# Kernel optimization log

Measured on AMD Instinct MI355X. Metric: run time of the kernel, lower is better.

Reference implementation:

```python
import jax, jax.numpy as jnp
import numpy as np
import math

# FPN level specs: (H, W, stride, anchor_size) for an 800x1216 input image
LEVELS = [(200, 304, 4, 32), (100, 152, 8, 64), (50, 76, 16, 128), (25, 38, 32, 256), (13, 19, 64, 512)]
RATIOS = (0.5, 1.0, 2.0)
A = 3
IMG_H, IMG_W = 800, 1216
PRE_NMS_TOPK = 1000   # test-time per level
POST_NMS_TOPK = 1000  # test-time
NMS_THRESH = 0.7
SCALE_CLAMP = math.log(1000.0 / 16)
NEG_INF = -1e9


def grid_anchors(H, W, stride, size):
    # detectron2 generate_cell_anchors: area=size^2, w=sqrt(area/r), h=w*r, centered at 0
    ca = []
    for r in RATIOS:
        w = math.sqrt(size * size / r)
        h = w * r
        ca.append([-w / 2.0, -h / 2.0, w / 2.0, h / 2.0])
    ca = np.asarray(ca, np.float32)                      # [A,4]
    sx = np.arange(W, dtype=np.float32) * stride
    sy = np.arange(H, dtype=np.float32) * stride
    yy, xx = np.meshgrid(sy, sx, indexing="ij")
    shifts = np.stack([xx, yy, xx, yy], -1).reshape(-1, 1, 4)  # [H*W,1,4]
    return jnp.asarray((shifts + ca[None]).reshape(-1, 4))      # [H*W*A,4]


def conv(x, w, b, pad):
    y = jax.lax.conv_general_dilated(x, w, (1, 1), [(pad, pad), (pad, pad)],
                                     dimension_numbers=("NCHW", "OIHW", "NCHW"))
    return y + b[None, :, None, None]


def apply_deltas(deltas, boxes):
    # Box2BoxTransform.apply_deltas with weights (1,1,1,1)
    w = boxes[..., 2] - boxes[..., 0]
    h = boxes[..., 3] - boxes[..., 1]
    cx = boxes[..., 0] + 0.5 * w
    cy = boxes[..., 1] + 0.5 * h
    dx, dy = deltas[..., 0], deltas[..., 1]
    dw = jnp.minimum(deltas[..., 2], SCALE_CLAMP)
    dh = jnp.minimum(deltas[..., 3], SCALE_CLAMP)
    pcx = dx * w + cx
    pcy = dy * h + cy
    pw = jnp.exp(dw) * w
    ph = jnp.exp(dh) * h
    return jnp.stack([pcx - 0.5 * pw, pcy - 0.5 * ph, pcx + 0.5 * pw, pcy + 0.5 * ph], -1)


def iou_one_vs_all(b, boxes):
    lt = jnp.maximum(b[:2], boxes[:, :2])
    rb = jnp.minimum(b[2:], boxes[:, 2:])
    wh = jnp.clip(rb - lt, 0.0)
    inter = wh[:, 0] * wh[:, 1]
    a1 = (b[2] - b[0]) * (b[3] - b[1])
    a2 = (boxes[:, 2] - boxes[:, 0]) * (boxes[:, 3] - boxes[:, 1])
    return inter / jnp.maximum(a1 + a2 - inter, 1e-9)


def nms_fixed(boxes, scores):
    # Fixed-iteration greedy NMS: POST_NMS_TOPK selections, jit-friendly.
    def body(scores_w, _):
        i = jnp.argmax(scores_w)
        s = scores_w[i]
        valid = s > NEG_INF / 2
        b = boxes[i]
        supp = iou_one_vs_all(b, boxes) > NMS_THRESH
        new_scores = jnp.where(supp, NEG_INF, scores_w)
        out_box = jnp.where(valid, b, jnp.zeros_like(b))
        out_s = jnp.where(valid, s, NEG_INF)
        return new_scores, (out_box, out_s)

    _, (kb, ks) = jax.lax.scan(body, scores, None, length=POST_NMS_TOPK)
    return kb, ks  # [K,4], [K]


def rpn_forward(feats, conv_w, conv_b, obj_w, obj_b, delta_w, delta_b):
    all_b, all_s = [], []
    for feat, (H, W, stride, size) in zip(feats, LEVELS):
        N = feat.shape[0]
        t = jax.nn.relu(conv(feat, conv_w, conv_b, 1))
        logits = conv(t, obj_w, obj_b, 0)                 # [N,A,H,W]
        deltas = conv(t, delta_w, delta_b, 0)             # [N,4A,H,W]
        logits = logits.transpose(0, 2, 3, 1).reshape(N, -1)                       # [N,HWA]
        deltas = deltas.reshape(N, A, 4, H, W).transpose(0, 3, 4, 1, 2).reshape(N, -1, 4)
        anch = grid_anchors(H, W, stride, size)           # [HWA,4]
        k = min(PRE_NMS_TOPK, H * W * A)
        s, idx = jax.lax.top_k(logits, k)                 # per-level pre-NMS topk
        d = jnp.take_along_axis(deltas, idx[..., None], axis=1)
        a = anch[idx]
        boxes = apply_deltas(d, a)
        boxes = jnp.stack([boxes[..., 0].clip(0, IMG_W), boxes[..., 1].clip(0, IMG_H),
                           boxes[..., 2].clip(0, IMG_W), boxes[..., 3].clip(0, IMG_H)], -1)
        all_b.append(boxes)
        all_s.append(s)
    boxes = jnp.concatenate(all_b, 1)   # [N,M,4]
    scores = jnp.concatenate(all_s, 1)  # [N,M]
    valid = ((boxes[..., 2] - boxes[..., 0]) > 0.0) & ((boxes[..., 3] - boxes[..., 1]) > 0.0)
    scores_m = jnp.where(valid, scores, NEG_INF)
    kb, ks = jax.vmap(nms_fixed)(boxes, scores_m)
    return jnp.concatenate([kb, ks[..., None]], -1)  # [N, POST_NMS_TOPK, 5]


def setup_inputs() -> dict:
    key = jax.random.key(0)
    ks = jax.random.split(key, 9)
    inp = {}
    for i, (name, (H, W, _, _)) in enumerate(zip(["feat_p2", "feat_p3", "feat_p4", "feat_p5", "feat_p6"], LEVELS)):
        inp[name] = jax.random.normal(ks[i], (2, 256, H, W), jnp.float32)
    inp["conv_w"] = jax.random.normal(ks[5], (256, 256, 3, 3), jnp.float32) * 0.02
    inp["conv_b"] = jnp.zeros((256,), jnp.float32)
    inp["obj_w"] = jax.random.normal(ks[6], (3, 256, 1, 1), jnp.float32) * 0.05
    inp["obj_b"] = jnp.zeros((3,), jnp.float32)
    inp["delta_w"] = jax.random.normal(ks[7], (12, 256, 1, 1), jnp.float32) * 0.02
    inp["delta_b"] = jnp.zeros((12,), jnp.float32)
    return inp


def reference(feat_p2, feat_p3, feat_p4, feat_p5, feat_p6, conv_w, conv_b, obj_w, obj_b, delta_w, delta_b):
    feats = [feat_p2, feat_p3, feat_p4, feat_p5, feat_p6]
    return rpn_forward(feats, conv_w, conv_b, obj_w, obj_b, delta_w, delta_b)
```

## Files before the change

### kernel.cpp

```cpp
#include <hip/hip_runtime.h>
#include <math.h>

typedef unsigned int u32;
typedef unsigned long long u64;
typedef __attribute__((ext_vector_type(8))) short bf16x8;
typedef __attribute__((ext_vector_type(4))) float f32x4;
typedef __attribute__((ext_vector_type(4))) double f64x4;

__constant__ int c_W[5]   = {304,152,76,38,19};
__constant__ int c_H[5]   = {200,100,50,25,13};
__constant__ int c_STR[5] = {4,8,16,32,64};
__constant__ int c_SZ[5]  = {32,64,128,256,512};
__constant__ int c_S[5]   = {182400,45600,11400,2850,741};
__constant__ int c_K1[5]  = {1024,1024,1024,1024,741};
__constant__ int c_K2[5]  = {1000,1000,1000,1000,741};
__constant__ u64 c_SCOFF[5] = {0,364800,456000,478800,484500};
__constant__ int c_LOFF[5] = {0,1000,2000,3000,4000};
__constant__ int c_PRE[6] = {0,2000,2600,2800,2850,2876};
__constant__ int c_NX[5]  = {5,3,2,1,1};

static const size_t h_SCOFF[5] = {0,364800,456000,478800,484500};

static constexpr size_t alignup(size_t x){ return (x + 255) & ~(size_t)255; }
static constexpr size_t N_SC   = 485982;
static constexpr int    M_CAND = 4741;
static constexpr size_t OFF_ASC   = 0;
static constexpr size_t OFF_THR   = alignup(OFF_ASC + N_SC*4);
static constexpr size_t OFF_QUOTA = OFF_THR + 64;
static constexpr size_t OFF_CNT   = OFF_QUOTA + 64;
static constexpr size_t OFF_SEL   = alignup(OFF_CNT + 256);
static constexpr size_t OFF_RSC   = alignup(OFF_SEL + 10*1024*4);
static constexpr size_t OFF_RDL   = alignup(OFF_RSC + 10*1024*8);
static constexpr size_t OFF_SORD  = alignup(OFF_RDL + 10*1024*4*8);
static constexpr size_t OFF_CBOX  = alignup(OFF_SORD + 10*1024*4);
static constexpr size_t OFF_CSC   = alignup(OFF_CBOX + 2ull*M_CAND*4*8);
static constexpr size_t OFF_SKEY  = alignup(OFF_CSC + 2ull*M_CAND*8);
static constexpr size_t OFF_SBOX  = alignup(OFF_SKEY + 2ull*8192*8);
static constexpr size_t OFF_SSC   = alignup(OFF_SBOX + 2ull*M_CAND*4*8);
static constexpr size_t OFF_MASK  = alignup(OFF_SSC + 2ull*M_CAND*8);
static constexpr size_t OFF_WB    = alignup(OFF_MASK + 2ull*4800*75*8);
static constexpr size_t OFF_WT    = alignup(OFF_WB + 589824ull*2);
static constexpr size_t WS_NEED   = OFF_WT + 589824ull*4;

__device__ __forceinline__ u64 ordkey(double s){
  u64 b = (u64)__double_as_longlong(s);
  return b ^ ((b >> 63) ? 0xFFFFFFFFFFFFFFFFULL : 0x8000000000000000ULL);
}
__device__ __forceinline__ u32 ordkey32(float s){
  u32 b = __float_as_uint(s);
  return b ^ ((b >> 31) ? 0xFFFFFFFFu : 0x80000000u);
}
__device__ __forceinline__ short bf16rne(float f){
  u32 u = __float_as_uint(f);
  u32 r = (u + 0x7FFFu + ((u >> 16) & 1u)) >> 16;
  return (short)r;
}

__global__ __launch_bounds__(256) void k_prep(const float* __restrict__ cw,
                                              short* __restrict__ wb2, float* __restrict__ wT,
                                              u32* cnt, u64* skey){
  int t = blockIdx.x*256 + threadIdx.x;
  if (t < 64) cnt[t] = 0;
  const int npad = 8192 - M_CAND;
  if (t < 2*npad){
    int img = t / npad;
    int j = M_CAND + (t - img*npad);
    skey[(size_t)img*8192 + j] = 0ULL;
  }
  {
    int ci = t & 31, n = (t >> 5) & 255, chunk = (t >> 13) & 7, tap = t >> 16;
    int cig = chunk*32 + ci;
    int ky = tap/3, kx = tap - ky*3;
    wb2[t] = bf16rne(cw[((size_t)(n*256 + cig)*3 + ky)*3 + kx]);
  }
  {
    int k = t >> 8, co = t & 255;
    wT[t] = cw[(size_t)co*2304 + k];
  }
}

__global__ __launch_bounds__(512) void k_convb(
    const float* __restrict__ f2, const float* __restrict__ f3,
    const float* __restrict__ f4, const float* __restrict__ f5,
    const float* __restrict__ f6, const short* __restrict__ wb2,
    const float* __restrict__ cb, const float* __restrict__ ow,
    const float* __restrict__ ob, float* __restrict__ ascore)
{
  __shared__ __align__(16) short Ap[198*136];
  __shared__ __align__(16) short Bt[256*40];
  __shared__ float ps[192];
  const int tid = threadIdx.x;
  int bid = blockIdx.x;
  int l = 0;
  while (bid >= c_PRE[l+1]) ++l;
  bid -= c_PRE[l];
  const int W = c_W[l], H = c_H[l], nx = c_NX[l];
  const int xb = bid % nx; int rem = bid / nx;
  const int y = rem % H; const int img = rem / H;
  const int x0 = xb*64;
  const size_t HW = (size_t)H*W;
  const float* fl = (l==0)?f2:(l==1)?f3:(l==2)?f4:(l==3)?f5:f6;
  const float* fb = fl + (size_t)img*256*HW;
  for (int e=tid;e<192;e+=512) ps[e]=0.f;

  const int wid = tid>>6, lane = tid&63;
  const int wr = wid>>2, wc = wid&3;
  const int l15 = lane&15, lg = lane>>4;

  f32x4 acc[2][4];
  #pragma unroll
  for(int a=0;a<2;a++)
    #pragma unroll
    for(int b=0;b<4;b++) acc[a][b] = (f32x4){0.f,0.f,0.f,0.f};

  for (int half=0; half<2; half++){
    __syncthreads();
    for (int e=tid; e<25344; e+=512){
      int ci = e/198, r = e - ci*198;
      int ry = r/66, cx = r - ry*66;
      int yy = y + ry - 1, xx = x0 + cx - 1;
      float v = 0.f;
      if (yy>=0 && yy<H && xx>=0 && xx<W)
        v = fb[(size_t)(half*128+ci)*HW + (size_t)yy*W + xx];
      Ap[r*136 + ci] = bf16rne(v);
    }
    for (int tap=0; tap<9; tap++){
      const int kyy = tap/3, kxx = tap - kyy*3;
      for (int c2=0; c2<4; c2++){
        __syncthreads();
        {
          const short* bs = wb2 + (((tap<<3) + (half<<2) + c2) << 13);
          for (int p=tid; p<1024; p+=512){
            int n = p>>2, seg = p&3;
            *(uint4*)(Bt + n*40 + (seg<<3)) = *(const uint4*)(bs + (n<<5) + (seg<<3));
          }
        }
        __syncthreads();
        const int colb = kyy*66 + wr*32 + l15 + kxx;
        const int cio  = c2*32 + lg*8;
        bf16x8 a0 = *(const bf16x8*)(Ap + colb*136 + cio);
        bf16x8 a1 = *(const bf16x8*)(Ap + (colb+16)*136 + cio);
        #pragma unroll
        for (int nf=0; nf<4; nf++){
          bf16x8 b = *(const bf16x8*)(Bt + (wc*64 + nf*16 + l15)*40 + lg*8);
          acc[0][nf] = __builtin_amdgcn_mfma_f32_16x16x32_bf16(a0, b, acc[0][nf], 0,0,0);
          acc[1][nf] = __builtin_amdgcn_mfma_f32_16x16x32_bf16(a1, b, acc[1][nf], 0,0,0);
        }
      }
    }
  }
  float p[3][2][4];
  #pragma unroll
  for (int a=0;a<3;a++)
    #pragma unroll
    for(int mf=0;mf<2;mf++)
      #pragma unroll
      for(int r=0;r<4;r++) p[a][mf][r]=0.f;
  #pragma unroll
  for (int nf=0; nf<4; nf++){
    int n = wc*64 + nf*16 + l15;
    float cbn = cb[n];
    float w0 = ow[n], w1 = ow[256+n], w2 = ow[512+n];
    #pragma unroll
    for (int mf=0; mf<2; mf++)
      #pragma unroll
      for (int r=0;r<4;r++){
        float t = acc[mf][nf][r] + cbn;
        t = t>0.f ? t : 0.f;
        p[0][mf][r] += w0*t; p[1][mf][r] += w1*t; p[2][mf][r] += w2*t;
      }
  }
  #pragma unroll
  for (int a=0;a<3;a++)
    #pragma unroll
    for (int mf=0;mf<2;mf++)
      #pragma unroll
      for (int r=0;r<4;r++){
        float v = p[a][mf][r];
        v += __shfl_xor(v, 1); v += __shfl_xor(v, 2);
        v += __shfl_xor(v, 4); v += __shfl_xor(v, 8);
        p[a][mf][r] = v;
      }
  if (l15 == 0){
    #pragma unroll
    for (int a=0;a<3;a++)
      #pragma unroll
      for (int mf=0;mf<2;mf++)
        #pragma unroll
        for (int r=0;r<4;r++)
          atomicAdd(&ps[a*64 + wr*32 + mf*16 + lg*4 + r], p[a][mf][r]);
  }
  __syncthreads();
  float* so = ascore + c_SCOFF[l] + (size_t)img*HW*3;
  for (int e=tid; e<192; e+=512){
    int a = e>>6, px = e&63;
    int xg = x0 + px;
    if (xg < W) so[((size_t)y*W + xg)*3 + a] = ps[e] + ob[a];
  }
}

__global__ __launch_bounds__(1024) void k_radix32(const float* __restrict__ ascore,
                                                  u32* __restrict__ thr, u32* __restrict__ quota)
{
  const int u = blockIdx.x, l = u >> 1, img = u & 1;
  const int n = c_S[l], k = c_K1[l];
  const int tid = threadIdx.x;
  if (n <= k){ if (tid==0){ thr[u]=0u; quota[u]=0xFFFFFFFFu; } return; }
  const float* sc = ascore + c_SCOFF[l] + (size_t)img*n;
  __shared__ u32 hist[2048];
  __shared__ u32 grp[32];
  __shared__ u32 s_pref;
  __shared__ u32 s_rem;
  if (tid==0){ s_pref=0u; s_rem=(u32)k; }
  const int shifts[3] = {21,10,0};
  const int bitsA[3]  = {11,11,10};
  for (int p=0;p<3;p++){
    const int nb = 1 << bitsA[p];
    for (int i=tid;i<nb;i+=1024) hist[i]=0u;
    __syncthreads();
    const u32 pref = s_pref;
    const int sh = shifts[p], hb = bitsA[p];
    for (int i=tid;i<n;i+=1024){
      u32 key = ordkey32(sc[i]);
      bool m = (p==0) || ((key >> (sh+hb)) == pref);
      if (m) atomicAdd(&hist[(key>>sh) & (u32)(nb-1)], 1u);
    }
    __syncthreads();
    const int per = nb >> 5;
    if (tid < 32){ u32 s=0; for (int q=0;q<per;q++) s += hist[tid*per+q]; grp[tid]=s; }
    __syncthreads();
    if (tid==0){
      u32 rem = s_rem, cum = 0;
      int g = 31;
      for (; g>0; g--){ if (cum + grp[g] >= rem) break; cum += grp[g]; }
      int b = (g+1)*per - 1;
      for (; b > g*per; b--){ if (cum + hist[b] >= rem) break; cum += hist[b]; }
      s_pref = (s_pref << hb) | (u32)b;
      s_rem = rem - cum;
    }
    __syncthreads();
  }
  if (tid==0){ thr[u] = s_pref; quota[u] = s_rem; }
}

__global__ __launch_bounds__(256) void k_compact32(const float* __restrict__ ascore,
    const u32* __restrict__ thr, const u32* __restrict__ quota,
    u32* __restrict__ cnt, u32* __restrict__ sel)
{
  const int u = blockIdx.y, l = u >> 1, img = u & 1;
  const int n = c_S[l];
  const int i = blockIdx.x*256 + threadIdx.x;
  if (i >= n) return;
  const float* sc = ascore + c_SCOFF[l] + (size_t)img*n;
  u32 key = ordkey32(sc[i]);
  u32 q = quota[u];
  bool take = false;
  if (q == 0xFFFFFFFFu) take = true;
  else {
    u32 t = thr[u];
    if (key > t) take = true;
    else if (key == t){ if (atomicAdd(&cnt[16+u],1u) < q) take = true; }
  }
  if (take){ u32 p = atomicAdd(&cnt[u],1u); if (p < 1024u) sel[u*1024 + p] = (u32)i; }
}

__global__ __launch_bounds__(256) void k_recompute(
    const float* __restrict__ f2, const float* __restrict__ f3,
    const float* __restrict__ f4, const float* __restrict__ f5,
    const float* __restrict__ f6,
    const float* __restrict__ wT, const float* __restrict__ cb,
    const float* __restrict__ ow, const float* __restrict__ ob,
    const float* __restrict__ dwt, const float* __restrict__ db,
    const u32* __restrict__ sel, const u32* __restrict__ cnt,
    double* __restrict__ rsc, double* __restrict__ rdl)
{
  const int u = blockIdx.y, l = u >> 1, img = u & 1;
  const int j0 = blockIdx.x * 16;
  const int cu = (int)cnt[u];
  if (j0 >= cu) return;
  const int W = c_W[l], H = c_H[l];
  const size_t HW = (size_t)W*H;
  const float* fl = (l==0)?f2:(l==1)?f3:(l==2)?f4:(l==3)?f5:f6;
  const float* fb = fl + (size_t)img*256*HW;
  __shared__ __align__(16) float spA[576*17];
  __shared__ int sx[16], sy[16], sa[16];
  const int tid = threadIdx.x;
  if (tid < 16){
    int j = j0 + tid; int ok = (j < cu) ? 1 : 0;
    u32 i = ok ? sel[u*1024 + j] : 0u;
    int pos = (int)(i/3u);
    sa[tid] = (int)i - pos*3; sx[tid] = pos % W; sy[tid] = pos / W;
  }
  const int wid = tid >> 6, lane = tid & 63;

  const f64x4 pz = (f64x4){0.0,0.0,0.0,0.0};
  f64x4 p1 = __builtin_amdgcn_mfma_f64_16x16x4f64((double)lane, 1.0, pz, 0,0,0);
  const double v0 = __shfl(p1[0], 0);
  const bool isA1 = (v0 > 50.0);
  const double aD = isA1 ? ((lane<16)?1.0:0.0) : (((lane&3)==0)?1.0:0.0);
  f64x4 p2 = __builtin_amdgcn_mfma_f64_16x16x4f64(aD, (double)lane, pz, 0,0,0);
  const bool own1 = (p2[0]==1.0)||(p2[1]==1.0)||(p2[2]==1.0)||(p2[3]==1.0);
  const bool isB1 = (__ballot(own1) != 0ull);
  const double aI = (double)(isA1 ? (lane&15) : (lane>>2));
  const double bD = isB1 ? ((lane<16)?1.0:0.0) : (((lane&3)==0)?1.0:0.0);
  f64x4 p3 = __builtin_amdgcn_mfma_f64_16x16x4f64(aI, bD, pz, 0,0,0);
  int row_[4], col_[4];
  const double cs = isB1 ? 1.0 : 0.25;
  #pragma unroll
  for (int r=0;r<4;r++){ col_[r] = (int)(p2[r]*cs); row_[r] = (int)p3[r]; }
  const int mrow = isA1 ? (lane&15) : (lane>>2);
  const int kA   = isA1 ? (lane>>4) : (lane&3);
  const int jB   = isB1 ? (lane&15) : (lane>>2);
  const int kB   = isB1 ? (lane>>4) : (lane&3);

  f64x4 acc[4];
  #pragma unroll
  for (int nt=0;nt<4;nt++) acc[nt] = pz;
  __syncthreads();
  for (int ci0=0; ci0<256; ci0+=64){
    for (int el=tid; el<9216; el+=256){
      int e = el/576, r = el - e*576;
      int ci = r/9, q = r - ci*9, ky = q/3, kx = q - ky*3;
      int yy = sy[e]+ky-1, xx = sx[e]+kx-1;
      float v = 0.0f;
      if (yy>=0 && yy<H && xx>=0 && xx<W) v = fb[(size_t)(ci0+ci)*HW + (size_t)yy*W + xx];
      spA[r*17 + e] = v;
    }
    __syncthreads();
    const float* wb = wT + (size_t)(ci0*9)*256 + (wid<<6) + jB;
    #pragma unroll 2
    for (int kt=0; kt<144; kt++){
      double a = (double)spA[(kt*4 + kA)*17 + mrow];
      const float* bp = wb + (size_t)(kt*4 + kB)*256;
      #pragma unroll
      for (int nt=0; nt<4; nt++){
        double b = (double)bp[nt*16];
        acc[nt] = __builtin_amdgcn_mfma_f64_16x16x4f64(a, b, acc[nt], 0,0,0);
      }
    }
    __syncthreads();
  }
  double* tl2 = (double*)spA;
  #pragma unroll
  for (int nt=0; nt<4; nt++){
    #pragma unroll
    for (int r=0;r<4;r++){
      const int co = (wid<<6) + nt*16 + col_[r];
      double t = acc[nt][r] + (double)cb[co];
      tl2[row_[r]*257 + co] = t > 0.0 ? t : 0.0;
    }
  }
  __syncthreads();
  if (tid < 80){
    int e = tid/5, q = tid - e*5;
    if (j0 + e < cu){
      int a = sa[e];
      const float* wv = (q==0) ? (ow + a*256) : (dwt + (size_t)(a*4 + q-1)*256);
      double bias = (q==0) ? (double)ob[a] : (double)db[a*4 + q-1];
      double s = 0.0;
      for (int c=0;c<256;c++) s += (double)wv[c]*tl2[e*257 + c];
      s += bias;
      int j = j0 + e;
      if (q==0) rsc[(size_t)u*1024 + j] = s;
      else      rdl[((size_t)u*1024 + j)*4 + (q-1)] = s;
    }
  }
}

__global__ __launch_bounds__(256) void k_sort1024(const double* __restrict__ rsc,
    const u32* __restrict__ cnt, u32* __restrict__ sord)
{
  const int u = blockIdx.x;
  const int cu = (int)cnt[u];
  const int tid = threadIdx.x;
  __shared__ u64 kk[1024];
  __shared__ u32 pp[1024];
  for (int i=tid;i<1024;i+=256){
    if (i < cu){ kk[i] = ordkey(rsc[(size_t)u*1024 + i]); pp[i] = (u32)i; }
    else       { kk[i] = 0ULL; pp[i] = 0xFFFFFFFFu; }
  }
  __syncthreads();
  for (int k=2;k<=1024;k<<=1){
    for (int j=k>>1;j>0;j>>=1){
      for (int i=tid;i<1024;i+=256){
        int l2 = i ^ j;
        if (l2 > i){
          u64 ka = kk[i], kb = kk[l2];
          u32 ia = pp[i], ib = pp[l2];
          bool before = (ka > kb) || (ka == kb && ia < ib);
          bool up = (i & k) == 0;
          if (up ? !before : before){
            kk[i]=kb; kk[l2]=ka; pp[i]=ib; pp[l2]=ia;
          }
        }
      }
      __syncthreads();
    }
  }
  for (int i=tid;i<1024;i+=256) sord[(size_t)u*1024 + i] = pp[i];
}

__global__ __launch_bounds__(256) void k_decode(
    const double* __restrict__ rsc, const double* __restrict__ rdl,
    const u32* __restrict__ sel, const u32* __restrict__ sord,
    double* __restrict__ cbox, double* __restrict__ csc,
    u64* __restrict__ skey, u32* __restrict__ cnt)
{
#pragma clang fp contract(off)
  const int u = blockIdx.y, l = u >> 1, img = u & 1;
  const int slot = blockIdx.x*256 + threadIdx.x;
  if (slot >= c_K2[l]) return;
  const u32 entry = sord[(size_t)u*1024 + slot];
  const u32 idx = sel[u*1024 + entry];
  const double s = rsc[(size_t)u*1024 + entry];
  const double d0 = rdl[((size_t)u*1024+entry)*4+0], d1 = rdl[((size_t)u*1024+entry)*4+1];
  double d2 = rdl[((size_t)u*1024+entry)*4+2], d3 = rdl[((size_t)u*1024+entry)*4+3];
  const int pos = (int)(idx/3u), a = (int)idx - pos*3;
  const int W = c_W[l];
  const int x = pos % W, y = pos / W;
  const double rr = (a==0) ? 0.5 : ((a==1) ? 1.0 : 2.0);
  const double sz = (double)c_SZ[l];
  const double wa = sqrt(sz*sz/rr);
  const double ha = wa*rr;
  const float xs = (float)(x*c_STR[l]);
  const float ys = (float)(y*c_STR[l]);
  const float ax0 = xs + (float)(-0.5*wa);
  const float ax1 = xs + (float)( 0.5*wa);
  const float ay0 = ys + (float)(-0.5*ha);
  const float ay1 = ys + (float)( 0.5*ha);
  const float wf = ax1 - ax0;
  const float hf = ay1 - ay0;
  const float cxf = ax0 + 0.5f*wf;
  const float cyf = ay0 + 0.5f*hf;
  const double Wd = (double)wf, Hd = (double)hf, CX = (double)cxf, CY = (double)cyf;
  const double SCLAMP = 4.135166556742356;
  if (d2 > SCLAMP) d2 = SCLAMP;
  if (d3 > SCLAMP) d3 = SCLAMP;
  double pcx = d0*Wd; pcx = pcx + CX;
  double pcy = d1*Hd; pcy = pcy + CY;
  const double pw = exp(d2)*Wd;
  const double ph = exp(d3)*Hd;
  double x0 = pcx - 0.5*pw;
  double y0 = pcy - 0.5*ph;
  double x1 = pcx + 0.5*pw;
  double y1 = pcy + 0.5*ph;
  x0 = fmin(fmax(x0, 0.0), 1216.0);
  x1 = fmin(fmax(x1, 0.0), 1216.0);
  y0 = fmin(fmax(y0, 0.0), 800.0);
  y1 = fmin(fmax(y1, 0.0), 800.0);
  const bool valid = (x1 - x0 > 0.0) && (y1 - y0 > 0.0);
  const double sm = valid ? s : -1e9;
  const int cp = c_LOFF[l] + slot;
  double* cb = cbox + ((size_t)img*M_CAND + cp)*4;
  cb[0]=x0; cb[1]=y0; cb[2]=x1; cb[3]=y1;
  csc[(size_t)img*M_CAND + cp] = sm;
  skey[(size_t)img*8192 + cp] = (ordkey(sm) & ~(u64)0x1FFF) | (u64)(8191 - cp);
  if (valid) atomicAdd(&cnt[32+img], 1u);
}

__global__ __launch_bounds__(1024) void k_sort(u64* __restrict__ key)
{
  const int img = blockIdx.x;
  u64* g = key + (size_t)img*8192;
  __shared__ u64 kk[8192];
  const int tid = threadIdx.x;
  for (int i=tid;i<8192;i+=1024) kk[i]=g[i];
  __syncthreads();
  for (int k=2;k<=8192;k<<=1){
    for (int j=k>>1;j>0;j>>=1){
      for (int i=tid;i<8192;i+=1024){
        int l = i ^ j;
        if (l > i){
          u64 ka = kk[i], kb = kk[l];
          bool before = (ka > kb);
          bool up = (i & k) == 0;
          if (up ? !before : before){ kk[i]=kb; kk[l]=ka; }
        }
      }
      __syncthreads();
    }
  }
  for (int i=tid;i<8192;i+=1024) g[i]=kk[i];
}

__global__ __launch_bounds__(256) void k_gather(const u64* __restrict__ skey,
    const double* __restrict__ cbox, const double* __restrict__ csc,
    double* __restrict__ sbox, double* __restrict__ ssc)
{
  int t = blockIdx.x*256 + threadIdx.x;
  if (t >= 2*M_CAND) return;
  int img = t / M_CAND, j = t - img*M_CAND;
  u32 b = 8191u - (u32)(skey[(size_t)img*8192 + j] & 0x1FFFull);
  const double* cb = cbox + ((size_t)img*M_CAND + b)*4;
  double* sb = sbox + ((size_t)img*M_CAND + j)*4;
  sb[0]=cb[0]; sb[1]=cb[1]; sb[2]=cb[2]; sb[3]=cb[3];
  ssc[(size_t)img*M_CAND + j] = csc[(size_t)img*M_CAND + b];
}

__global__ __launch_bounds__(256) void k_iou(const double* __restrict__ sbox, u64* __restrict__ mask)
{
#pragma clang fp contract(off)
  const int jb = blockIdx.x, ib = blockIdx.y, img = blockIdx.z;
  if (jb < ib) return;
  __shared__ double ibx[64][4];
  const int tid = threadIdx.x;
  const int lane = tid & 63, wv = tid >> 6;
  if (tid < 64){
    int ig = ib*64 + tid;
    if (ig < M_CAND){
      const double* b = sbox + ((size_t)img*M_CAND + ig)*4;
      ibx[tid][0]=b[0]; ibx[tid][1]=b[1]; ibx[tid][2]=b[2]; ibx[tid][3]=b[3];
    } else { ibx[tid][0]=0; ibx[tid][1]=0; ibx[tid][2]=0; ibx[tid][3]=0; }
  }
  const int jg = jb*64 + lane;
  double jx0=0,jy0=0,jx1=0,jy1=0;
  if (jg < M_CAND){
    const double* b = sbox + ((size_t)img*M_CAND + jg)*4;
    jx0=b[0]; jy0=b[1]; jx1=b[2]; jy1=b[3];
  }
  const double ja = (jx1-jx0)*(jy1-jy0);
  __syncthreads();
  for (int s=0;s<16;s++){
    const int il = wv*16 + s;
    const int ig = ib*64 + il;
    double bx0=ibx[il][0], by0=ibx[il][1], bx1=ibx[il][2], by1=ibx[il][3];
    double lt0 = bx0 > jx0 ? bx0 : jx0;
    double lt1 = by0 > jy0 ? by0 : jy0;
    double rb0 = bx1 < jx1 ? bx1 : jx1;
    double rb1 = by1 < jy1 ? by1 : jy1;
    double w = rb0-lt0; if (w<0.0) w=0.0;
    double h = rb1-lt1; if (h<0.0) h=0.0;
    double inter = w*h;
    double ia = (bx1-bx0)*(by1-by0);
    double un = ia + ja - inter; if (un < 1e-9) un = 1e-9;
    bool bit = (jg > ig) && (jg < M_CAND) && (inter/un > 0.7);
    u64 m = __ballot(bit);
    if (lane == 0) mask[((size_t)img*4800 + ig)*75 + jb] = m;
  }
}

__global__ __launch_bounds__(256) void k_nms(const u64* __restrict__ mask,
    const double* __restrict__ sbox, const double* __restrict__ ssc,
    const u32* __restrict__ cnt, float* __restrict__ out)
{
  const int img = blockIdx.x;
  const int tid = threadIdx.x;
  __shared__ u64 remv[75];
  __shared__ u64 diag[64];
  __shared__ int keep[1000];
  __shared__ int ck[64];
  __shared__ int s_kc, s_nk, s_done;
  if (tid < 75) remv[tid] = 0ULL;
  if (tid == 0){ s_kc = 0; s_done = 0; }
  int vc = (int)cnt[32+img]; if (vc > M_CAND) vc = M_CAND;
  const u64* mrow = mask + (size_t)img*4800*75;
  __syncthreads();
  for (int c=0; c<75; c++){
    if (c*64 >= vc) break;
    if (tid < 64) diag[tid] = mrow[(size_t)(c*64+tid)*75 + c];
    __syncthreads();
    if (tid == 0){
      u64 w = remv[c];
      int kc = s_kc, nk = 0;
      int lim = vc - c*64; if (lim > 64) lim = 64;
      for (int k=0;k<lim;k++){
        if (!((w >> k) & 1ULL)){
          int idx = c*64 + k;
          keep[kc] = idx;
          ck[nk++] = idx;
          kc++;
          if (kc >= 1000) break;
          w |= diag[k];
        }
      }
      s_kc = kc; s_nk = nk;
      if (kc >= 1000) s_done = 1;
    }
    __syncthreads();
    if (s_done) break;
    const int nk = s_nk;
    if (nk > 0){
      for (int c2 = c+1+tid; c2 < 75; c2 += 256){
        u64 a = remv[c2];
        for (int q=0;q<nk;q++) a |= mrow[(size_t)ck[q]*75 + c2];
        remv[c2] = a;
      }
    }
    __syncthreads();
  }
  __syncthreads();
  int kc = s_kc; if (kc > 1000) kc = 1000;
  for (int r = tid; r < 1000; r += 256){
    float v0=0.f,v1=0.f,v2=0.f,v3=0.f,v4=-1e9f;
    if (r < kc){
      int idx = keep[r];
      const double* b = sbox + ((size_t)img*M_CAND + idx)*4;
      v0=(float)b[0]; v1=(float)b[1]; v2=(float)b[2]; v3=(float)b[3];
      v4=(float)ssc[(size_t)img*M_CAND + idx];
    }
    float* o = out + ((size_t)img*1000 + r)*5;
    o[0]=v0; o[1]=v1; o[2]=v2; o[3]=v3; o[4]=v4;
  }
}

extern "C" void kernel_launch(void* const* d_in, const int* in_sizes, int n_in,
                              void* d_out, int out_size, void* d_ws, size_t ws_size,
                              hipStream_t stream)
{
  const float* feat[5];
  for (int i=0;i<5;i++) feat[i] = (const float*)d_in[i];
  const float* cw  = (const float*)d_in[5];
  const float* cb  = (const float*)d_in[6];
  const float* ow  = (const float*)d_in[7];
  const float* ob  = (const float*)d_in[8];
  const float* dwt = (const float*)d_in[9];
  const float* db  = (const float*)d_in[10];
  float* out = (float*)d_out;
  char* ws = (char*)d_ws;
  if (ws_size < WS_NEED) return;

  float*  ascore = (float*)(ws + OFF_ASC);
  u32*    thr    = (u32*)(ws + OFF_THR);
  u32*    quota  = (u32*)(ws + OFF_QUOTA);
  u32*    cnt    = (u32*)(ws + OFF_CNT);
  u32*    sel    = (u32*)(ws + OFF_SEL);
  double* rsc    = (double*)(ws + OFF_RSC);
  double* rdl    = (double*)(ws + OFF_RDL);
  u32*    sord   = (u32*)(ws + OFF_SORD);
  double* cbox   = (double*)(ws + OFF_CBOX);
  double* csc    = (double*)(ws + OFF_CSC);
  u64*    skey   = (u64*)(ws + OFF_SKEY);
  double* sbox   = (double*)(ws + OFF_SBOX);
  double* ssc    = (double*)(ws + OFF_SSC);
  u64*    mask   = (u64*)(ws + OFF_MASK);
  short*  wb2    = (short*)(ws + OFF_WB);
  float*  wT     = (float*)(ws + OFF_WT);

  k_prep<<<2304,256,0,stream>>>(cw, wb2, wT, cnt, skey);
  k_convb<<<2876,512,0,stream>>>(feat[0],feat[1],feat[2],feat[3],feat[4],
                                 wb2, cb, ow, ob, ascore);
  k_radix32<<<10,1024,0,stream>>>(ascore, thr, quota);
  k_compact32<<<dim3(713,10),256,0,stream>>>(ascore, thr, quota, cnt, sel);
  k_recompute<<<dim3(64,10),256,0,stream>>>(feat[0],feat[1],feat[2],feat[3],feat[4],
                                            wT, cb, ow, ob, dwt, db, sel, cnt, rsc, rdl);
  k_sort1024<<<10,256,0,stream>>>(rsc, cnt, sord);
  k_decode<<<dim3(4,10),256,0,stream>>>(rsc, rdl, sel, sord, cbox, csc, skey, cnt);
  k_sort<<<2,1024,0,stream>>>(skey);
  k_gather<<<38,256,0,stream>>>(skey, cbox, csc, sbox, ssc);
  k_iou<<<dim3(75,75,2),256,0,stream>>>(sbox, mask);
  k_nms<<<2,256,0,stream>>>(mask, sbox, ssc, cnt, out);
}
```

Baseline: 1.825 ms.

## Load conv weights directly from global, swizzle LDS activation tile, drop per-chunk barriers

The conv kernel no longer stages weight chunks through shared memory with two barriers per chunk. Each lane now reads its weight fragments straight from global memory, which is likely L2-resident. The activation tile is stored with an XOR swizzle and no padding, and is filled two channels at a time with packed 32-bit writes. This removes 72 barrier pairs per half and cuts LDS footprint, but adds more global loads per wave and relies on cache hits for the weights.

```diff
diff --git a/kernel.cpp b/kernel.cpp
--- a/kernel.cpp
+++ b/kernel.cpp
@@ -86,8 +86,7 @@
     const float* __restrict__ cb, const float* __restrict__ ow,
     const float* __restrict__ ob, float* __restrict__ ascore)
 {
-  __shared__ __align__(16) short Ap[198*136];
-  __shared__ __align__(16) short Bt[256*40];
+  __shared__ __align__(16) short Ap[198*128];
   __shared__ float ps[192];
   const int tid = threadIdx.x;
   int bid = blockIdx.x;
@@ -115,37 +114,42 @@
 
   for (int half=0; half<2; half++){
     __syncthreads();
-    for (int e=tid; e<25344; e+=512){
-      int ci = e/198, r = e - ci*198;
+    for (int e=tid; e<12672; e+=512){
+      int cp = e/198, r = e - cp*198;
+      int ci = cp<<1;
       int ry = r/66, cx = r - ry*66;
       int yy = y + ry - 1, xx = x0 + cx - 1;
-      float v = 0.f;
-      if (yy>=0 && yy<H && xx>=0 && xx<W)
-        v = fb[(size_t)(half*128+ci)*HW + (size_t)yy*W + xx];
-      Ap[r*136 + ci] = bf16rne(v);
-    }
+      float v0 = 0.f, v1 = 0.f;
+      if (yy>=0 && yy<H && xx>=0 && xx<W){
+        const float* fp = fb + (size_t)(half*128+ci)*HW + (size_t)yy*W + xx;
+        v0 = fp[0]; v1 = fp[HW];
+      }
+      u32 pk = (u32)(unsigned short)bf16rne(v0) | ((u32)(unsigned short)bf16rne(v1) << 16);
+      int pos = (((ci>>3) ^ (r&7))<<3) + (ci&7);
+      *(u32*)(Ap + r*128 + pos) = pk;
+    }
+    __syncthreads();
     for (int tap=0; tap<9; tap++){
       const int kyy = tap/3, kxx = tap - kyy*3;
+      #pragma unroll
       for (int c2=0; c2<4; c2++){
-        __syncthreads();
-        {
-          const short* bs = wb2 + (((tap<<3) + (half<<2) + c2) << 13);
-          for (int p=tid; p<1024; p+=512){
-            int n = p>>2, seg = p&3;
-            *(uint4*)(Bt + n*40 + (seg<<3)) = *(const uint4*)(bs + (n<<5) + (seg<<3));
-          }
-        }
-        __syncthreads();
+        const short* bs = wb2 + (((tap<<3) + (half<<2) + c2) << 13) + (lg<<3);
+        bf16x8 b0 = *(const bf16x8*)(bs + ((wc*64 +  0 + l15)<<5));
+        bf16x8 b1 = *(const bf16x8*)(bs + ((wc*64 + 16 + l15)<<5));
+        bf16x8 b2 = *(const bf16x8*)(bs + ((wc*64 + 32 + l15)<<5));
+        bf16x8 b3 = *(const bf16x8*)(bs + ((wc*64 + 48 + l15)<<5));
         const int colb = kyy*66 + wr*32 + l15 + kxx;
-        const int cio  = c2*32 + lg*8;
-        bf16x8 a0 = *(const bf16x8*)(Ap + colb*136 + cio);
-        bf16x8 a1 = *(const bf16x8*)(Ap + (colb+16)*136 + cio);
-        #pragma unroll
-        for (int nf=0; nf<4; nf++){
-          bf16x8 b = *(const bf16x8*)(Bt + (wc*64 + nf*16 + l15)*40 + lg*8);
-          acc[0][nf] = __builtin_amdgcn_mfma_f32_16x16x32_bf16(a0, b, acc[0][nf], 0,0,0);
-          acc[1][nf] = __builtin_amdgcn_mfma_f32_16x16x32_bf16(a1, b, acc[1][nf], 0,0,0);
-        }
+        const int swz = (((c2<<2) + lg) ^ (colb&7)) << 3;
+        bf16x8 a0 = *(const bf16x8*)(Ap + colb*128 + swz);
+        bf16x8 a1 = *(const bf16x8*)(Ap + (colb+16)*128 + swz);
+        acc[0][0] = __builtin_amdgcn_mfma_f32_16x16x32_bf16(a0, b0, acc[0][0], 0,0,0);
+        acc[1][0] = __builtin_amdgcn_mfma_f32_16x16x32_bf16(a1, b0, acc[1][0], 0,0,0);
+        acc[0][1] = __builtin_amdgcn_mfma_f32_16x16x32_bf16(a0, b1, acc[0][1], 0,0,0);
+        acc[1][1] = __builtin_amdgcn_mfma_f32_16x16x32_bf16(a1, b1, acc[1][1], 0,0,0);
+        acc[0][2] = __builtin_amdgcn_mfma_f32_16x16x32_bf16(a0, b2, acc[0][2], 0,0,0);
+        acc[1][2] = __builtin_amdgcn_mfma_f32_16x16x32_bf16(a1, b2, acc[1][2], 0,0,0);
+        acc[0][3] = __builtin_amdgcn_mfma_f32_16x16x32_bf16(a0, b3, acc[0][3], 0,0,0);
+        acc[1][3] = __builtin_amdgcn_mfma_f32_16x16x32_bf16(a1, b3, acc[1][3], 0,0,0);
       }
     }
   }
```

Result: faster. 1.668 ms (-8.6%).
